# Performance work log

Measured on AMD Instinct MI355X. Metric: run time of the kernel, lower is better.

Reference implementation:

```python
import jax, jax.numpy as jnp
import numpy as np
from jax import lax

HOPS = 3
B, L, D = 16, 512, 768


def _softmask(x, mask):
    # x: [B,L,L] scores, mask: [B,L] {0,1} floats. Scaled masked softmax per RACL softmask_2d.
    x = x - jnp.max(x, axis=-1, keepdims=True)
    y = jnp.exp(x) * mask[:, None, :]          # mask keys
    att = y / (jnp.sum(y, axis=-1, keepdims=True) + 1e-10)
    return att * mask[:, :, None]              # mask queries


def _conv1d(x, w, b):
    # x: [B,L,D]; w: [D_out, D_in, 3]; conv over L with padding 1 (same length).
    out = lax.conv_general_dilated(jnp.transpose(x, (0, 2, 1)), w, (1,), [(1, 1)],
                                   dimension_numbers=('NCH', 'OIH', 'NCH'))
    return jnp.transpose(out + b[None, :, None], (0, 2, 1))


def _l2norm(x):
    # F.normalize(p=2, dim=-1) with eps=1e-12 (clamp_min)
    return x / jnp.maximum(jnp.linalg.norm(x, axis=-1, keepdims=True), 1e-12)


def setup_inputs() -> dict:
    key = jax.random.key(0)
    ks = jax.random.split(key, 8)
    inputs = jax.random.normal(ks[0], (B, L, D), dtype=jnp.float32)
    mask = jnp.ones((B, L), dtype=jnp.float32)
    conv_w = jax.random.normal(ks[1], (HOPS, D, D, 3), dtype=jnp.float32) * 0.02
    conv_b = jax.random.normal(ks[2], (HOPS, D), dtype=jnp.float32) * 0.02
    pool_w1 = jax.random.normal(ks[3], (D, D), dtype=jnp.float32) * 0.02
    pool_b1 = jax.random.normal(ks[4], (D,), dtype=jnp.float32) * 0.02
    pool_w2 = jax.random.normal(ks[5], (D,), dtype=jnp.float32) * 0.02
    pool_b2 = jax.random.normal(ks[6], (1,), dtype=jnp.float32) * 0.02
    position = jnp.zeros((B, L), dtype=jnp.int64)  # unused by the module
    return {"inputs": inputs, "mask": mask, "conv_w": conv_w, "conv_b": conv_b,
            "pool_w1": pool_w1, "pool_b1": pool_b1, "pool_w2": pool_w2,
            "pool_b2": pool_b2, "position": position}


def reference(inputs, mask, conv_w, conv_b, pool_w1, pool_b1, pool_w2, pool_b2, position):
    att_out = []
    # hop 0: raw (un-normalized) similarity on inputs
    see = jnp.einsum('bld,bmd->blm', inputs, inputs)
    att_out.append(jnp.einsum('blm,bmd->bld', _softmask(see, mask), inputs)[:, :, None, :])
    cur = inputs
    for h in range(HOPS):
        conv = jax.nn.relu(_conv1d(cur, conv_w[h], conv_b[h]))  # dropout = identity (eval)
        n = _l2norm(conv)
        att = _softmask(jnp.einsum('bld,bmd->blm', n, n), mask)  # cosine-sim attention
        att_out.append(jnp.einsum('blm,bmd->bld', att, conv)[:, :, None, :])
        cur = conv
    result = jnp.concatenate(att_out, axis=-2)  # [B,L,HOPS+1,D]
    hidden = jnp.tanh(jnp.einsum('blhd,de->blhe', result, pool_w1) + pool_b1)
    scores = jnp.einsum('blhd,d->blh', hidden, pool_w2) + pool_b2  # [B,L,HOPS+1]
    att_w = jax.nn.softmax(scores, axis=-1)
    weighted = jnp.einsum('blh,blhd->bld', att_w, result)
    return cur, weighted
```

## Files before the change

### kernel.cpp

```cpp
#include <hip/hip_runtime.h>
#include <math.h>

#define B_ 16
#define L_ 512
#define D_ 768
#define HOPS_ 3
#define LK 64

typedef __attribute__((ext_vector_type(8))) short s16x8;
typedef __attribute__((ext_vector_type(4))) short s16x4;
typedef __attribute__((ext_vector_type(4))) float f32x4;

typedef __attribute__((address_space(1))) const unsigned gu32;
typedef __attribute__((address_space(3))) unsigned lu32;

__device__ __forceinline__ void gl16(const void* g, void* l) {
  __builtin_amdgcn_global_load_lds((gu32*)g, (lu32*)l, 16, 0, 0);
}

__device__ __forceinline__ short f2bf(float f) {
  unsigned u = __float_as_uint(f);
  unsigned r = (u + 0x7fffu + ((u >> 16) & 1u)) >> 16;
  return (short)r;
}
__device__ __forceinline__ float bf2f(short s) {
  unsigned u = ((unsigned)(unsigned short)s) << 16;
  return __uint_as_float(u);
}
__device__ __forceinline__ float tanh_fast(float x) {
  float e = __expf(2.f * x);
  return 1.f - 2.f / (e + 1.f);
}

__device__ __forceinline__ s16x8* lds_slot(short (*T)[LK], int row, int slot) {
  return (s16x8*)&T[row][(slot ^ (row & 7)) * 8];
}

__device__ __forceinline__ void mfma4(short (*As)[LK], short (*Bs)[LK],
                                      f32x4 acc[4][4], int wr, int wc, int lq, int lr) {
#pragma unroll
  for (int ks = 0; ks < 2; ++ks) {
    int sl = ks * 4 + lq;
    s16x8 av[4], bv[4];
#pragma unroll
    for (int m = 0; m < 4; ++m) av[m] = *lds_slot(As, wr * 64 + m * 16 + lr, sl);
#pragma unroll
    for (int n = 0; n < 4; ++n) bv[n] = *lds_slot(Bs, wc * 64 + n * 16 + lr, sl);
#pragma unroll
    for (int m = 0; m < 4; ++m)
#pragma unroll
      for (int n = 0; n < 4; ++n)
        acc[m][n] = __builtin_amdgcn_mfma_f32_16x16x32_bf16(av[m], bv[n], acc[m][n], 0, 0, 0);
  }
}

__device__ __forceinline__ void mfma2(short (*As)[LK], short (*Bs)[LK],
                                      f32x4 acc[2][4], int wr, int wc, int lq, int lr) {
#pragma unroll
  for (int ks = 0; ks < 2; ++ks) {
    int sl = ks * 4 + lq;
    s16x8 av[2], bv[4];
#pragma unroll
    for (int m = 0; m < 2; ++m) av[m] = *lds_slot(As, wr * 32 + m * 16 + lr, sl);
#pragma unroll
    for (int n = 0; n < 4; ++n) bv[n] = *lds_slot(Bs, wc * 64 + n * 16 + lr, sl);
#pragma unroll
    for (int m = 0; m < 2; ++m)
#pragma unroll
      for (int n = 0; n < 4; ++n)
        acc[m][n] = __builtin_amdgcn_mfma_f32_16x16x32_bf16(av[m], bv[n], acc[m][n], 0, 0, 0);
  }
}

__device__ __forceinline__ int xcd_remap(int bid, int n) {
  return (bid & 7) * (n >> 3) + (bid >> 3);
}

template <int SPLIT>
__global__ __launch_bounds__(256) void k_sim_mfma(const short* __restrict__ X,
                                                  float* __restrict__ Sout) {
  int wg = xcd_remap(blockIdx.x, gridDim.x);
  int jb = wg & 3, ib = (wg >> 2) & 7, b = wg >> 5;
  int i0 = ib * 64, j0 = jb * 128;
  const int ld = SPLIT ? 1536 : D_;
  const short* Xb = X + (size_t)b * L_ * ld;
  int t = threadIdx.x, lane = t & 63, wid = t >> 6;
  int wr = wid >> 1, wc = wid & 1, lq = lane >> 4, lr = lane & 15;
  __shared__ short As[64][LK];
  __shared__ short Bs[128][LK];
  f32x4 acc[2][4];
#pragma unroll
  for (int m = 0; m < 2; ++m)
#pragma unroll
    for (int n = 0; n < 4; ++n) acc[m][n] = (f32x4){0.f, 0.f, 0.f, 0.f};
  int lrow = lane >> 3;
  int sw = ((lane & 7) ^ lrow) * 8;
  const short* apg[2];
  const short* bpg[4];
#pragma unroll
  for (int j = 0; j < 2; ++j)
    apg[j] = Xb + (size_t)(i0 + wid * 16 + j * 8 + lrow) * ld + sw;
#pragma unroll
  for (int j = 0; j < 4; ++j)
    bpg[j] = Xb + (size_t)(j0 + wid * 32 + j * 8 + lrow) * ld + sw;

  const int K = SPLIT ? 2304 : D_;
  for (int k0 = 0; k0 < K; k0 += LK) {
    int seg = SPLIT ? (k0 / 768) : 0;
    int kl = k0 - seg * 768;
    int ak = kl + ((SPLIT && seg == 1) ? 768 : 0);
    int bk = kl + ((SPLIT && seg == 2) ? 768 : 0);
#pragma unroll
    for (int j = 0; j < 2; ++j) gl16(apg[j] + ak, &As[wid * 16 + j * 8][0]);
#pragma unroll
    for (int j = 0; j < 4; ++j) gl16(bpg[j] + bk, &Bs[wid * 32 + j * 8][0]);
    __syncthreads();
    mfma2(As, Bs, acc, wr, wc, lq, lr);
    __syncthreads();
  }
  float* Cb = Sout + (size_t)b * L_ * L_;
#pragma unroll
  for (int m = 0; m < 2; ++m)
#pragma unroll
    for (int n = 0; n < 4; ++n)
#pragma unroll
      for (int rr = 0; rr < 4; ++rr)
        Cb[(size_t)(i0 + wr * 32 + m * 16 + 4 * lq + rr) * L_ +
           (j0 + wc * 64 + n * 16 + lr)] = acc[m][n][rr];
}

template <int WF32>
__global__ __launch_bounds__(256) void k_conv_mfma(const short* __restrict__ X, int ldx,
                                                   const short* __restrict__ Wt2,
                                                   const float* __restrict__ bias,
                                                   short* __restrict__ Ybf,
                                                   float* __restrict__ Yf,
                                                   float* __restrict__ rnsq,
                                                   const short* __restrict__ zbuf,
                                                   short* __restrict__ Vt) {
  int wg = xcd_remap(blockIdx.x, gridDim.x);
  int ob = wg % 6;
  int m_ = wg / 6;
  int b = m_ >> 2, l0 = (m_ & 3) * 128, o0 = ob * 128;
  const short* Xb = X + (size_t)b * L_ * ldx;
  int t = threadIdx.x, lane = t & 63, wid = t >> 6;
  int wr = wid >> 1, wc = wid & 1, lq = lane >> 4, lr = lane & 15;
  __shared__ short smem[17408];
  short (*As)[LK] = (short(*)[LK])smem;
  short (*Bs)[LK] = (short(*)[LK])(smem + 128 * LK);
  f32x4 acc[4][4];
#pragma unroll
  for (int m = 0; m < 4; ++m)
#pragma unroll
    for (int n = 0; n < 4; ++n) acc[m][n] = (f32x4){0.f, 0.f, 0.f, 0.f};
  int lrow = lane >> 3;
  int sw = ((lane & 7) ^ lrow) * 8;
  int arow[4];
  const short* bpg[4];
#pragma unroll
  for (int j = 0; j < 4; ++j) {
    arow[j] = l0 + wid * 32 + j * 8 + lrow;
    bpg[j] = Wt2 + (size_t)(o0 + wid * 32 + j * 8 + lrow) * (3 * D_) + sw;
  }
  const short* zp = zbuf + sw;

  for (int k0 = 0; k0 < 3 * D_; k0 += LK) {
    int tap = k0 / D_;
    int kl = k0 - tap * D_;
#pragma unroll
    for (int j = 0; j < 4; ++j) {
      int l = arow[j] + tap - 1;
      const short* src =
          ((unsigned)l < (unsigned)L_) ? Xb + (size_t)l * ldx + kl + sw : zp;
      gl16(src, &As[wid * 32 + j * 8][0]);
    }
#pragma unroll
    for (int j = 0; j < 4; ++j) gl16(bpg[j] + k0, &Bs[wid * 32 + j * 8][0]);
    __syncthreads();
    mfma4(As, Bs, acc, wr, wc, lq, lr);
    __syncthreads();
  }
  float bv[4];
#pragma unroll
  for (int n = 0; n < 4; ++n) bv[n] = bias[o0 + wc * 64 + n * 16 + lr];
#pragma unroll
  for (int m = 0; m < 4; ++m)
#pragma unroll
    for (int n = 0; n < 4; ++n)
#pragma unroll
      for (int rr = 0; rr < 4; ++rr)
        acc[m][n][rr] = fmaxf(acc[m][n][rr] + bv[n], 0.f);
#pragma unroll
  for (int m = 0; m < 4; ++m)
#pragma unroll
    for (int rr = 0; rr < 4; ++rr) {
      int l = l0 + wr * 64 + m * 16 + 4 * lq + rr;
      size_t rowoff = ((size_t)b * L_ + l) * D_;
      float ss = 0.f;
#pragma unroll
      for (int n = 0; n < 4; ++n) {
        int o = o0 + wc * 64 + n * 16 + lr;
        float v = acc[m][n][rr];
        Ybf[rowoff + o] = f2bf(v);
        if (WF32) Yf[rowoff + o] = v;
        ss += v * v;
      }
      ss += __shfl_xor(ss, 1);
      ss += __shfl_xor(ss, 2);
      ss += __shfl_xor(ss, 4);
      ss += __shfl_xor(ss, 8);
      if (lr == 0) atomicAdd(&rnsq[(size_t)b * L_ + l], ss);
    }
  short (*T)[136] = (short(*)[136])smem;
#pragma unroll
  for (int m = 0; m < 4; ++m)
#pragma unroll
    for (int n = 0; n < 4; ++n) {
      int o_ = wc * 64 + n * 16 + lr;
      int lb = wr * 64 + m * 16 + 4 * lq;
      s16x4 pk;
#pragma unroll
      for (int rr = 0; rr < 4; ++rr) pk[rr] = f2bf(acc[m][n][rr]);
      *(s16x4*)&T[o_][lb] = pk;
    }
  __syncthreads();
  short* Vtb = Vt + (size_t)b * D_ * L_;
#pragma unroll
  for (int p = 0; p < 8; ++p) {
    int dl = p * 16 + (t >> 4), lc = (t & 15) * 8;
    s16x8 q = *(const s16x8*)&T[dl][lc];
    *(s16x8*)&Vtb[(size_t)(o0 + dl) * L_ + l0 + lc] = q;
  }
}

__global__ __launch_bounds__(256) void k_att_mfma(const short* __restrict__ P,
                                                  const short* __restrict__ Vt,
                                                  short* __restrict__ Rb, int hop) {
  int wg = xcd_remap(blockIdx.x, gridDim.x);
  int db = wg % 6;
  int r2 = wg / 6;
  int b = r2 >> 2, i0 = (r2 & 3) * 128, d0 = db * 128;
  const short* Pb = P + (size_t)b * L_ * L_;
  const short* Vb = Vt + (size_t)b * D_ * L_;
  int t = threadIdx.x, lane = t & 63, wid = t >> 6;
  int wr = wid >> 1, wc = wid & 1, lq = lane >> 4, lr = lane & 15;
  __shared__ short As[128][LK];
  __shared__ short Bs[128][LK];
  f32x4 acc[4][4];
#pragma unroll
  for (int m = 0; m < 4; ++m)
#pragma unroll
    for (int n = 0; n < 4; ++n) acc[m][n] = (f32x4){0.f, 0.f, 0.f, 0.f};
  int lrow = lane >> 3;
  int sw = ((lane & 7) ^ lrow) * 8;
  const short* apg[4];
  const short* bpg[4];
#pragma unroll
  for (int j = 0; j < 4; ++j) {
    apg[j] = Pb + (size_t)(i0 + wid * 32 + j * 8 + lrow) * L_ + sw;
    bpg[j] = Vb + (size_t)(d0 + wid * 32 + j * 8 + lrow) * L_ + sw;
  }
  for (int k0 = 0; k0 < L_; k0 += LK) {
#pragma unroll
    for (int j = 0; j < 4; ++j) gl16(apg[j] + k0, &As[wid * 32 + j * 8][0]);
#pragma unroll
    for (int j = 0; j < 4; ++j) gl16(bpg[j] + k0, &Bs[wid * 32 + j * 8][0]);
    __syncthreads();
    mfma4(As, Bs, acc, wr, wc, lq, lr);
    __syncthreads();
  }
#pragma unroll
  for (int m = 0; m < 4; ++m)
#pragma unroll
    for (int n = 0; n < 4; ++n)
#pragma unroll
      for (int rr = 0; rr < 4; ++rr) {
        int i = i0 + wr * 64 + m * 16 + 4 * lq + rr;
        int d = d0 + wc * 64 + n * 16 + lr;
        Rb[((size_t)(b * L_ + i) * 4 + hop) * D_ + d] = f2bf(acc[m][n][rr]);
      }
}

__global__ __launch_bounds__(256) void k_pool_mfma(const short* __restrict__ Rb,
                                                   const short* __restrict__ W1t,
                                                   const float* __restrict__ b1,
                                                   const float* __restrict__ w2,
                                                   float* __restrict__ ps) {
  int wg = xcd_remap(blockIdx.x, gridDim.x);
  int eb = wg % 6;
  int r0 = (wg / 6) * 128, e0 = eb * 128;
  int t = threadIdx.x, lane = t & 63, wid = t >> 6;
  int wr = wid >> 1, wc = wid & 1, lq = lane >> 4, lr = lane & 15;
  __shared__ short As[128][LK];
  __shared__ short Bs[128][LK];
  f32x4 acc[4][4];
#pragma unroll
  for (int m = 0; m < 4; ++m)
#pragma unroll
    for (int n = 0; n < 4; ++n) acc[m][n] = (f32x4){0.f, 0.f, 0.f, 0.f};
  int lrow = lane >> 3;
  int sw = ((lane & 7) ^ lrow) * 8;
  const short* apg[4];
  const short* bpg[4];
#pragma unroll
  for (int j = 0; j < 4; ++j) {
    apg[j] = Rb + (size_t)(r0 + wid * 32 + j * 8 + lrow) * D_ + sw;
    bpg[j] = W1t + (size_t)(e0 + wid * 32 + j * 8 + lrow) * D_ + sw;
  }
  for (int k0 = 0; k0 < D_; k0 += LK) {
#pragma unroll
    for (int j = 0; j < 4; ++j) gl16(apg[j] + k0, &As[wid * 32 + j * 8][0]);
#pragma unroll
    for (int j = 0; j < 4; ++j) gl16(bpg[j] + k0, &Bs[wid * 32 + j * 8][0]);
    __syncthreads();
    mfma4(As, Bs, acc, wr, wc, lq, lr);
    __syncthreads();
  }
  float b1v[4], w2v[4];
#pragma unroll
  for (int n = 0; n < 4; ++n) {
    int e = e0 + wc * 64 + n * 16 + lr;
    b1v[n] = b1[e];
    w2v[n] = w2[e];
  }
#pragma unroll
  for (int m = 0; m < 4; ++m)
#pragma unroll
    for (int rr = 0; rr < 4; ++rr) {
      float p = 0.f;
#pragma unroll
      for (int n = 0; n < 4; ++n) p += tanh_fast(acc[m][n][rr] + b1v[n]) * w2v[n];
      p += __shfl_xor(p, 1);
      p += __shfl_xor(p, 2);
      p += __shfl_xor(p, 4);
      p += __shfl_xor(p, 8);
      if (lr == 0) atomicAdd(&ps[r0 + wr * 64 + m * 16 + 4 * lq + rr], p);
    }
}

__global__ __launch_bounds__(256) void k_prep2(const float* __restrict__ in,
                                               short* __restrict__ Xs,
                                               short* __restrict__ Vt) {
  int l0 = blockIdx.x * 32, d0 = blockIdx.y * 32, b = blockIdx.z;
  __shared__ short tile[32][40];
  int r = threadIdx.x >> 5, c = threadIdx.x & 31;
  const float* ib = in + ((size_t)b * L_ + l0) * D_ + d0;
#pragma unroll
  for (int i = 0; i < 4; ++i) {
    int rr = r + 8 * i;
    float x = ib[(size_t)rr * D_ + c];
    short hi = f2bf(x);
    short lo = f2bf(x - bf2f(hi));
    size_t bl = (size_t)b * L_ + l0 + rr;
    Xs[bl * 1536 + d0 + c] = hi;
    Xs[bl * 1536 + 768 + d0 + c] = lo;
    tile[c][rr] = hi;
  }
  __syncthreads();
  int dl = threadIdx.x >> 3, lc = (threadIdx.x & 7) * 4;
  s16x4 q = *(const s16x4*)&tile[dl][lc];
  *(s16x4*)&Vt[((size_t)b * D_ + d0 + dl) * L_ + l0 + lc] = q;
}

__global__ void k_wprep(const float* __restrict__ w, const float* __restrict__ W1,
                        short* __restrict__ Wt2, short* __restrict__ W1t) {
  size_t idx = (size_t)blockIdx.x * 256 + threadIdx.x;
  const size_t tot1 = (size_t)HOPS_ * D_ * 3 * D_;
  if (idx < tot1) {
    int i = (int)(idx % D_);
    size_t tmp = idx / D_;
    int kk = (int)(tmp % 3);
    tmp /= 3;
    int o = (int)(tmp % D_);
    int h = (int)(tmp / D_);
    Wt2[idx] = f2bf(w[(((size_t)h * D_ + o) * D_ + i) * 3 + kk]);
  } else {
    size_t i2 = idx - tot1;
    if (i2 >= (size_t)D_ * D_) return;
    int e = (int)(i2 / D_), d = (int)(i2 % D_);
    W1t[i2] = f2bf(W1[(size_t)d * D_ + e]);
  }
}

template <int NORM>
__global__ __launch_bounds__(256) void k_softmask3(const float* __restrict__ S,
                                                   const float* __restrict__ mask,
                                                   const float* __restrict__ rsq,
                                                   short* __restrict__ P) {
  int b = blockIdx.y;
  int i = blockIdx.x * 4 + (threadIdx.x >> 6);
  int l = threadIdx.x & 63;
  const float* row = S + ((size_t)b * L_ + i) * L_;
  const float* mb = mask + (size_t)b * L_;
  float v[8], mk[8];
  {
    float4 s0 = ((const float4*)row)[l * 2];
    float4 s1 = ((const float4*)row)[l * 2 + 1];
    float4 m0 = ((const float4*)mb)[l * 2];
    float4 m1 = ((const float4*)mb)[l * 2 + 1];
    v[0] = s0.x; v[1] = s0.y; v[2] = s0.z; v[3] = s0.w;
    v[4] = s1.x; v[5] = s1.y; v[6] = s1.z; v[7] = s1.w;
    mk[0] = m0.x; mk[1] = m0.y; mk[2] = m0.z; mk[3] = m0.w;
    mk[4] = m1.x; mk[5] = m1.y; mk[6] = m1.z; mk[7] = m1.w;
  }
  if (NORM) {
    float ri = 1.f / fmaxf(sqrtf(rsq[(size_t)b * L_ + i]), 1e-12f);
    const float4* rq = (const float4*)(rsq + (size_t)b * L_);
    float4 q0 = rq[l * 2], q1 = rq[l * 2 + 1];
    float qq[8] = {q0.x, q0.y, q0.z, q0.w, q1.x, q1.y, q1.z, q1.w};
#pragma unroll
    for (int e = 0; e < 8; ++e) v[e] *= ri / fmaxf(sqrtf(qq[e]), 1e-12f);
  }
  float m = v[0];
#pragma unroll
  for (int e = 1; e < 8; ++e) m = fmaxf(m, v[e]);
#pragma unroll
  for (int s = 1; s < 64; s <<= 1) m = fmaxf(m, __shfl_xor(m, s));
  float y[8], sum = 0.f;
#pragma unroll
  for (int e = 0; e < 8; ++e) {
    y[e] = __expf(v[e] - m) * mk[e];
    sum += y[e];
  }
#pragma unroll
  for (int s = 1; s < 64; s <<= 1) sum += __shfl_xor(sum, s);
  float inv = mb[i] / (sum + 1e-10f);
  s16x8 pk;
#pragma unroll
  for (int e = 0; e < 8; ++e) pk[e] = f2bf(y[e] * inv);
  ((s16x8*)(P + ((size_t)b * L_ + i) * L_))[l] = pk;
}

__global__ __launch_bounds__(256) void k_weighted2(const short* __restrict__ Rb,
                                                   const float* __restrict__ ps,
                                                   float* __restrict__ out) {
  int b = blockIdx.y, l = blockIdx.x;
  size_t bl = (size_t)b * L_ + l;
  const float* p = ps + bl * 4;
  float s0 = p[0], s1 = p[1], s2 = p[2], s3 = p[3];
  float m = fmaxf(fmaxf(s0, s1), fmaxf(s2, s3));
  float e0 = __expf(s0 - m), e1 = __expf(s1 - m), e2 = __expf(s2 - m),
        e3 = __expf(s3 - m);
  float inv = 1.f / (e0 + e1 + e2 + e3);
  e0 *= inv; e1 *= inv; e2 *= inv; e3 *= inv;
  const short* Rrow = Rb + bl * 4 * D_;
  float* orow = out + bl * D_;
  for (int d = threadIdx.x; d < D_; d += 256) {
    orow[d] = e0 * bf2f(Rrow[d]) + e1 * bf2f(Rrow[D_ + d]) +
              e2 * bf2f(Rrow[2 * D_ + d]) + e3 * bf2f(Rrow[3 * D_ + d]);
  }
}

extern "C" void kernel_launch(void* const* d_in, const int* in_sizes, int n_in,
                              void* d_out, int out_size, void* d_ws, size_t ws_size,
                              hipStream_t stream) {
  const float* inputs  = (const float*)d_in[0];
  const float* mask    = (const float*)d_in[1];
  const float* conv_w  = (const float*)d_in[2];
  const float* conv_b  = (const float*)d_in[3];
  const float* pool_w1 = (const float*)d_in[4];
  const float* pool_b1 = (const float*)d_in[5];
  const float* pool_w2 = (const float*)d_in[6];
  float* out = (float*)d_out;

  const size_t BLD = (size_t)B_ * L_ * D_;
  const size_t BLL = (size_t)B_ * L_ * L_;
  const size_t BL  = (size_t)B_ * L_;

  char* w = (char*)d_ws;
  short* Xs   = (short*)w; w += (size_t)2 * BLD * 2;
  short* Wt2  = (short*)w; w += (size_t)HOPS_ * 3 * D_ * D_ * 2;
  short* W1t  = (short*)w; w += (size_t)D_ * D_ * 2;
  float* S    = (float*)w; w += BLL * 4;
  short* Pb   = (short*)w; w += BLL * 2;
  short* YbfA = (short*)w; w += BLD * 2;
  short* YbfB = (short*)w; w += BLD * 2;
  short* Vt   = (short*)w; w += BLD * 2;
  short* Rb   = (short*)w; w += 4 * BLD * 2;
  float* ps   = (float*)w; w += BL * 4 * 4;
  float* rnsq = (float*)w; w += BL * 3 * 4;
  short* zbuf = (short*)w; w += 1024;
  const size_t zero_bytes = BL * 4 * 4 + BL * 3 * 4 + 1024;

  hipMemsetAsync(ps, 0, zero_bytes, stream);

  dim3 gpre(L_ / 32, D_ / 32, B_);
  dim3 gsm(L_ / 4, B_);
  dim3 grow(L_, B_);
  const int GSIM = (L_ / 64) * (L_ / 128) * B_;
  const int GCONV = (D_ / 128) * (L_ / 128) * B_;
  const int GATT = GCONV;
  const int GPOOL = (D_ / 128) * (4 * B_ * L_ / 128);
  const size_t wtot = (size_t)HOPS_ * D_ * 3 * D_ + (size_t)D_ * D_;

  k_prep2<<<gpre, 256, 0, stream>>>(inputs, Xs, Vt);
  k_wprep<<<dim3((unsigned)((wtot + 255) / 256)), 256, 0, stream>>>(conv_w, pool_w1,
                                                                     Wt2, W1t);

  k_sim_mfma<1><<<GSIM, 256, 0, stream>>>(Xs, S);
  k_softmask3<0><<<gsm, 256, 0, stream>>>(S, mask, nullptr, Pb);
  k_att_mfma<<<GATT, 256, 0, stream>>>(Pb, Vt, Rb, 0);

  const short* cur = Xs;
  int ldc = 1536;
  for (int h = 0; h < HOPS_; ++h) {
    short* cv = (h & 1) ? YbfB : YbfA;
    const short* Wh = Wt2 + (size_t)h * 3 * D_ * D_;
    const float* bh = conv_b + (size_t)h * D_;
    float* rq = rnsq + (size_t)h * BL;
    if (h == HOPS_ - 1)
      k_conv_mfma<1><<<GCONV, 256, 0, stream>>>(cur, ldc, Wh, bh, cv, out, rq, zbuf, Vt);
    else
      k_conv_mfma<0><<<GCONV, 256, 0, stream>>>(cur, ldc, Wh, bh, cv, nullptr, rq, zbuf, Vt);
    k_sim_mfma<0><<<GSIM, 256, 0, stream>>>(cv, S);
    k_softmask3<1><<<gsm, 256, 0, stream>>>(S, mask, rq, Pb);
    k_att_mfma<<<GATT, 256, 0, stream>>>(Pb, Vt, Rb, h + 1);
    cur = cv;
    ldc = D_;
  }

  k_pool_mfma<<<GPOOL, 256, 0, stream>>>(Rb, W1t, pool_b1, pool_w2, ps);
  k_weighted2<<<grow, 256, 0, stream>>>(Rb, ps, out + BLD);
}
```

Measured before the change: 483.0 us.

## Fuse similarity GEMM with masked softmax into one kernel producing bf16 probabilities

Replaces the separate similarity GEMM (which wrote fp32 scores to global memory) and the row-softmax kernel with one kernel. Each 512-thread block computes full 32x512 score rows and does the max/sum reductions in registers and LDS, then writes bf16 probabilities directly. This removes the fp32 score round trip and four kernel launches. The cost is fewer, larger blocks (256 total) with a K-step of 32 and more barriers, which may reduce occupancy and MFMA efficiency. The final weighted-sum kernel is also vectorised to process two rows per block with 16-byte loads.

```diff
diff --git a/kernel.cpp b/kernel.cpp
--- a/kernel.cpp
+++ b/kernel.cpp
@@ -54,79 +54,159 @@
   }
 }
 
-__device__ __forceinline__ void mfma2(short (*As)[LK], short (*Bs)[LK],
-                                      f32x4 acc[2][4], int wr, int wc, int lq, int lr) {
-#pragma unroll
-  for (int ks = 0; ks < 2; ++ks) {
-    int sl = ks * 4 + lq;
-    s16x8 av[2], bv[4];
-#pragma unroll
-    for (int m = 0; m < 2; ++m) av[m] = *lds_slot(As, wr * 32 + m * 16 + lr, sl);
-#pragma unroll
-    for (int n = 0; n < 4; ++n) bv[n] = *lds_slot(Bs, wc * 64 + n * 16 + lr, sl);
-#pragma unroll
-    for (int m = 0; m < 2; ++m)
-#pragma unroll
-      for (int n = 0; n < 4; ++n)
-        acc[m][n] = __builtin_amdgcn_mfma_f32_16x16x32_bf16(av[m], bv[n], acc[m][n], 0, 0, 0);
-  }
-}
-
 __device__ __forceinline__ int xcd_remap(int bid, int n) {
   return (bid & 7) * (n >> 3) + (bid >> 3);
 }
 
-template <int SPLIT>
-__global__ __launch_bounds__(256) void k_sim_mfma(const short* __restrict__ X,
-                                                  float* __restrict__ Sout) {
+template <int SPLIT, int NORM>
+__global__ __launch_bounds__(512) void k_simsm(const short* __restrict__ X,
+                                               const float* __restrict__ mask,
+                                               const float* __restrict__ rsq,
+                                               short* __restrict__ P) {
   int wg = xcd_remap(blockIdx.x, gridDim.x);
-  int jb = wg & 3, ib = (wg >> 2) & 7, b = wg >> 5;
-  int i0 = ib * 64, j0 = jb * 128;
+  int ib = wg & 15, b = wg >> 4;
+  int i0 = ib * 32;
   const int ld = SPLIT ? 1536 : D_;
   const short* Xb = X + (size_t)b * L_ * ld;
-  int t = threadIdx.x, lane = t & 63, wid = t >> 6;
-  int wr = wid >> 1, wc = wid & 1, lq = lane >> 4, lr = lane & 15;
-  __shared__ short As[64][LK];
-  __shared__ short Bs[128][LK];
+  int t = threadIdx.x, lane = t & 63, w = t >> 6;
+  int lq = lane >> 4, lr = lane & 15;
+  __shared__ __align__(16) short smem[17408];
+  short (*As)[32] = (short(*)[32])smem;
+  short (*Bs)[32] = (short(*)[32])(smem + 1024);
   f32x4 acc[2][4];
 #pragma unroll
   for (int m = 0; m < 2; ++m)
 #pragma unroll
     for (int n = 0; n < 4; ++n) acc[m][n] = (f32x4){0.f, 0.f, 0.f, 0.f};
-  int lrow = lane >> 3;
-  int sw = ((lane & 7) ^ lrow) * 8;
-  const short* apg[2];
-  const short* bpg[4];
-#pragma unroll
-  for (int j = 0; j < 2; ++j)
-    apg[j] = Xb + (size_t)(i0 + wid * 16 + j * 8 + lrow) * ld + sw;
-#pragma unroll
-  for (int j = 0; j < 4; ++j)
-    bpg[j] = Xb + (size_t)(j0 + wid * 32 + j * 8 + lrow) * ld + sw;
+
+  int rl = lane >> 2;
+  int ss = ((lane & 3) ^ ((lane >> 3) & 3)) * 8;
+  int wa = (w < 2) ? w : 0;
+  const short* asrc = Xb + (size_t)(i0 + wa * 16 + rl) * ld + ss;
+  short* adst = &As[wa * 16][0];
+  const short* bsrc[4];
+  short* bdst[4];
+#pragma unroll
+  for (int jj = 0; jj < 4; ++jj) {
+    int r0 = jj * 128 + w * 16;
+    bsrc[jj] = Xb + (size_t)(r0 + rl) * ld + ss;
+    bdst[jj] = &Bs[r0][0];
+  }
+  int so = (lq ^ ((lr >> 1) & 3)) * 8;
 
   const int K = SPLIT ? 2304 : D_;
-  for (int k0 = 0; k0 < K; k0 += LK) {
+  for (int k0 = 0; k0 < K; k0 += 32) {
     int seg = SPLIT ? (k0 / 768) : 0;
     int kl = k0 - seg * 768;
     int ak = kl + ((SPLIT && seg == 1) ? 768 : 0);
     int bk = kl + ((SPLIT && seg == 2) ? 768 : 0);
-#pragma unroll
-    for (int j = 0; j < 2; ++j) gl16(apg[j] + ak, &As[wid * 16 + j * 8][0]);
-#pragma unroll
-    for (int j = 0; j < 4; ++j) gl16(bpg[j] + bk, &Bs[wid * 32 + j * 8][0]);
-    __syncthreads();
-    mfma2(As, Bs, acc, wr, wc, lq, lr);
-    __syncthreads();
-  }
-  float* Cb = Sout + (size_t)b * L_ * L_;
+    if (w < 2) gl16(asrc + ak, adst);
+#pragma unroll
+    for (int jj = 0; jj < 4; ++jj) gl16(bsrc[jj] + bk, bdst[jj]);
+    __syncthreads();
+    s16x8 av[2], bv[4];
+#pragma unroll
+    for (int m = 0; m < 2; ++m) av[m] = *(const s16x8*)&As[m * 16 + lr][so];
+#pragma unroll
+    for (int n = 0; n < 4; ++n) bv[n] = *(const s16x8*)&Bs[w * 64 + n * 16 + lr][so];
+#pragma unroll
+    for (int m = 0; m < 2; ++m)
+#pragma unroll
+      for (int n = 0; n < 4; ++n)
+        acc[m][n] = __builtin_amdgcn_mfma_f32_16x16x32_bf16(av[m], bv[n], acc[m][n], 0, 0, 0);
+    __syncthreads();
+  }
+
+  const float* mb = mask + (size_t)b * L_;
+  const float* rqb = rsq + (size_t)b * L_;
+  float mk_j[4], inv_rj[4];
+#pragma unroll
+  for (int n = 0; n < 4; ++n) {
+    int col = w * 64 + n * 16 + lr;
+    mk_j[n] = mb[col];
+    if (NORM) inv_rj[n] = 1.f / fmaxf(sqrtf(rqb[col]), 1e-12f);
+  }
+  float mk_i[2][4], inv_ri[2][4], rmax[2][4];
 #pragma unroll
   for (int m = 0; m < 2; ++m)
 #pragma unroll
-    for (int n = 0; n < 4; ++n)
+    for (int rr = 0; rr < 4; ++rr) {
+      int row = m * 16 + lq * 4 + rr;
+      mk_i[m][rr] = mb[i0 + row];
+      if (NORM) inv_ri[m][rr] = 1.f / fmaxf(sqrtf(rqb[i0 + row]), 1e-12f);
+      float vmx = -3.4e38f;
+#pragma unroll
+      for (int n = 0; n < 4; ++n) {
+        float v = acc[m][n][rr];
+        if (NORM) v *= inv_ri[m][rr] * inv_rj[n];
+        acc[m][n][rr] = v;
+        vmx = fmaxf(vmx, v);
+      }
+#pragma unroll
+      for (int s = 1; s < 16; s <<= 1) vmx = fmaxf(vmx, __shfl_xor(vmx, s));
+      rmax[m][rr] = vmx;
+    }
+  float* red = (float*)smem;
+  float* rowred = red + 256;
+  if (lr == 0) {
+#pragma unroll
+    for (int m = 0; m < 2; ++m)
 #pragma unroll
       for (int rr = 0; rr < 4; ++rr)
-        Cb[(size_t)(i0 + wr * 32 + m * 16 + 4 * lq + rr) * L_ +
-           (j0 + wc * 64 + n * 16 + lr)] = acc[m][n][rr];
+        red[w * 32 + m * 16 + lq * 4 + rr] = rmax[m][rr];
+  }
+  __syncthreads();
+  if (t < 32) {
+    float mx = red[t];
+#pragma unroll
+    for (int ww = 1; ww < 8; ++ww) mx = fmaxf(mx, red[ww * 32 + t]);
+    rowred[t] = mx;
+  }
+  __syncthreads();
+  float rsum[2][4];
+#pragma unroll
+  for (int m = 0; m < 2; ++m)
+#pragma unroll
+    for (int rr = 0; rr < 4; ++rr) {
+      float M = rowred[m * 16 + lq * 4 + rr];
+      float s = 0.f;
+#pragma unroll
+      for (int n = 0; n < 4; ++n) {
+        float y = __expf(acc[m][n][rr] - M) * mk_j[n];
+        acc[m][n][rr] = y;
+        s += y;
+      }
+#pragma unroll
+      for (int sh = 1; sh < 16; sh <<= 1) s += __shfl_xor(s, sh);
+      rsum[m][rr] = s;
+    }
+  __syncthreads();
+  if (lr == 0) {
+#pragma unroll
+    for (int m = 0; m < 2; ++m)
+#pragma unroll
+      for (int rr = 0; rr < 4; ++rr)
+        red[w * 32 + m * 16 + lq * 4 + rr] = rsum[m][rr];
+  }
+  __syncthreads();
+  if (t < 32) {
+    float s = red[t];
+#pragma unroll
+    for (int ww = 1; ww < 8; ++ww) s += red[ww * 32 + t];
+    rowred[t] = s;
+  }
+  __syncthreads();
+  short* Pb = P + ((size_t)b * L_ + i0) * L_;
+#pragma unroll
+  for (int m = 0; m < 2; ++m)
+#pragma unroll
+    for (int rr = 0; rr < 4; ++rr) {
+      int row = m * 16 + lq * 4 + rr;
+      float inv = mk_i[m][rr] / (rowred[row] + 1e-10f);
+#pragma unroll
+      for (int n = 0; n < 4; ++n)
+        Pb[(size_t)row * L_ + w * 64 + n * 16 + lr] = f2bf(acc[m][n][rr] * inv);
+    }
 }
 
 template <int WF32>
@@ -145,7 +225,7 @@
   const short* Xb = X + (size_t)b * L_ * ldx;
   int t = threadIdx.x, lane = t & 63, wid = t >> 6;
   int wr = wid >> 1, wc = wid & 1, lq = lane >> 4, lr = lane & 15;
-  __shared__ short smem[17408];
+  __shared__ __align__(16) short smem[17408];
   short (*As)[LK] = (short(*)[LK])smem;
   short (*Bs)[LK] = (short(*)[LK])(smem + 128 * LK);
   f32x4 acc[4][4];
@@ -244,8 +324,8 @@
   const short* Vb = Vt + (size_t)b * D_ * L_;
   int t = threadIdx.x, lane = t & 63, wid = t >> 6;
   int wr = wid >> 1, wc = wid & 1, lq = lane >> 4, lr = lane & 15;
-  __shared__ short As[128][LK];
-  __shared__ short Bs[128][LK];
+  __shared__ __align__(16) short As[128][LK];
+  __shared__ __align__(16) short Bs[128][LK];
   f32x4 acc[4][4];
 #pragma unroll
   for (int m = 0; m < 4; ++m)
@@ -291,8 +371,8 @@
   int r0 = (wg / 6) * 128, e0 = eb * 128;
   int t = threadIdx.x, lane = t & 63, wid = t >> 6;
   int wr = wid >> 1, wc = wid & 1, lq = lane >> 4, lr = lane & 15;
-  __shared__ short As[128][LK];
-  __shared__ short Bs[128][LK];
+  __shared__ __align__(16) short As[128][LK];
+  __shared__ __align__(16) short Bs[128][LK];
   f32x4 acc[4][4];
 #pragma unroll
   for (int m = 0; m < 4; ++m)
@@ -382,60 +462,13 @@
   }
 }
 
-template <int NORM>
-__global__ __launch_bounds__(256) void k_softmask3(const float* __restrict__ S,
-                                                   const float* __restrict__ mask,
-                                                   const float* __restrict__ rsq,
-                                                   short* __restrict__ P) {
-  int b = blockIdx.y;
-  int i = blockIdx.x * 4 + (threadIdx.x >> 6);
-  int l = threadIdx.x & 63;
-  const float* row = S + ((size_t)b * L_ + i) * L_;
-  const float* mb = mask + (size_t)b * L_;
-  float v[8], mk[8];
-  {
-    float4 s0 = ((const float4*)row)[l * 2];
-    float4 s1 = ((const float4*)row)[l * 2 + 1];
-    float4 m0 = ((const float4*)mb)[l * 2];
-    float4 m1 = ((const float4*)mb)[l * 2 + 1];
-    v[0] = s0.x; v[1] = s0.y; v[2] = s0.z; v[3] = s0.w;
-    v[4] = s1.x; v[5] = s1.y; v[6] = s1.z; v[7] = s1.w;
-    mk[0] = m0.x; mk[1] = m0.y; mk[2] = m0.z; mk[3] = m0.w;
-    mk[4] = m1.x; mk[5] = m1.y; mk[6] = m1.z; mk[7] = m1.w;
-  }
-  if (NORM) {
-    float ri = 1.f / fmaxf(sqrtf(rsq[(size_t)b * L_ + i]), 1e-12f);
-    const float4* rq = (const float4*)(rsq + (size_t)b * L_);
-    float4 q0 = rq[l * 2], q1 = rq[l * 2 + 1];
-    float qq[8] = {q0.x, q0.y, q0.z, q0.w, q1.x, q1.y, q1.z, q1.w};
-#pragma unroll
-    for (int e = 0; e < 8; ++e) v[e] *= ri / fmaxf(sqrtf(qq[e]), 1e-12f);
-  }
-  float m = v[0];
-#pragma unroll
-  for (int e = 1; e < 8; ++e) m = fmaxf(m, v[e]);
-#pragma unroll
-  for (int s = 1; s < 64; s <<= 1) m = fmaxf(m, __shfl_xor(m, s));
-  float y[8], sum = 0.f;
-#pragma unroll
-  for (int e = 0; e < 8; ++e) {
-    y[e] = __expf(v[e] - m) * mk[e];
-    sum += y[e];
-  }
-#pragma unroll
-  for (int s = 1; s < 64; s <<= 1) sum += __shfl_xor(sum, s);
-  float inv = mb[i] / (sum + 1e-10f);
-  s16x8 pk;
-#pragma unroll
-  for (int e = 0; e < 8; ++e) pk[e] = f2bf(y[e] * inv);
-  ((s16x8*)(P + ((size_t)b * L_ + i) * L_))[l] = pk;
-}
-
 __global__ __launch_bounds__(256) void k_weighted2(const short* __restrict__ Rb,
                                                    const float* __restrict__ ps,
                                                    float* __restrict__ out) {
-  int b = blockIdx.y, l = blockIdx.x;
-  size_t bl = (size_t)b * L_ + l;
+  if (threadIdx.x >= 192) return;
+  int rowl = threadIdx.x / 96;
+  int ln = threadIdx.x % 96;
+  size_t bl = (size_t)blockIdx.x * 2 + rowl;
   const float* p = ps + bl * 4;
   float s0 = p[0], s1 = p[1], s2 = p[2], s3 = p[3];
   float m = fmaxf(fmaxf(s0, s1), fmaxf(s2, s3));
@@ -444,11 +477,22 @@
   float inv = 1.f / (e0 + e1 + e2 + e3);
   e0 *= inv; e1 *= inv; e2 *= inv; e3 *= inv;
   const short* Rrow = Rb + bl * 4 * D_;
-  float* orow = out + bl * D_;
-  for (int d = threadIdx.x; d < D_; d += 256) {
-    orow[d] = e0 * bf2f(Rrow[d]) + e1 * bf2f(Rrow[D_ + d]) +
-              e2 * bf2f(Rrow[2 * D_ + d]) + e3 * bf2f(Rrow[3 * D_ + d]);
-  }
+  int d = ln * 8;
+  s16x8 r0 = *(const s16x8*)&Rrow[d];
+  s16x8 r1 = *(const s16x8*)&Rrow[D_ + d];
+  s16x8 r2 = *(const s16x8*)&Rrow[2 * D_ + d];
+  s16x8 r3 = *(const s16x8*)&Rrow[3 * D_ + d];
+  float* orow = out + bl * D_ + d;
+  float4 o0, o1;
+  float* ov[2] = {&o0.x, &o1.x};
+#pragma unroll
+  for (int e = 0; e < 8; ++e) {
+    float v = e0 * bf2f(r0[e]) + e1 * bf2f(r1[e]) + e2 * bf2f(r2[e]) +
+              e3 * bf2f(r3[e]);
+    ov[e >> 2][e & 3] = v;
+  }
+  ((float4*)orow)[0] = o0;
+  ((float4*)orow)[1] = o1;
 }
 
 extern "C" void kernel_launch(void* const* d_in, const int* in_sizes, int n_in,
@@ -471,7 +515,6 @@
   short* Xs   = (short*)w; w += (size_t)2 * BLD * 2;
   short* Wt2  = (short*)w; w += (size_t)HOPS_ * 3 * D_ * D_ * 2;
   short* W1t  = (short*)w; w += (size_t)D_ * D_ * 2;
-  float* S    = (float*)w; w += BLL * 4;
   short* Pb   = (short*)w; w += BLL * 2;
   short* YbfA = (short*)w; w += BLD * 2;
   short* YbfB = (short*)w; w += BLD * 2;
@@ -485,9 +528,7 @@
   hipMemsetAsync(ps, 0, zero_bytes, stream);
 
   dim3 gpre(L_ / 32, D_ / 32, B_);
-  dim3 gsm(L_ / 4, B_);
-  dim3 grow(L_, B_);
-  const int GSIM = (L_ / 64) * (L_ / 128) * B_;
+  const int GSIM = (L_ / 32) * B_;
   const int GCONV = (D_ / 128) * (L_ / 128) * B_;
   const int GATT = GCONV;
   const int GPOOL = (D_ / 128) * (4 * B_ * L_ / 128);
@@ -497,8 +538,7 @@
   k_wprep<<<dim3((unsigned)((wtot + 255) / 256)), 256, 0, stream>>>(conv_w, pool_w1,
                                                                      Wt2, W1t);
 
-  k_sim_mfma<1><<<GSIM, 256, 0, stream>>>(Xs, S);
-  k_softmask3<0><<<gsm, 256, 0, stream>>>(S, mask, nullptr, Pb);
+  k_simsm<1, 0><<<GSIM, 512, 0, stream>>>(Xs, mask, rnsq, Pb);
   k_att_mfma<<<GATT, 256, 0, stream>>>(Pb, Vt, Rb, 0);
 
   const short* cur = Xs;
@@ -512,13 +552,12 @@
       k_conv_mfma<1><<<GCONV, 256, 0, stream>>>(cur, ldc, Wh, bh, cv, out, rq, zbuf, Vt);
     else
       k_conv_mfma<0><<<GCONV, 256, 0, stream>>>(cur, ldc, Wh, bh, cv, nullptr, rq, zbuf, Vt);
-    k_sim_mfma<0><<<GSIM, 256, 0, stream>>>(cv, S);
-    k_softmask3<1><<<gsm, 256, 0, stream>>>(S, mask, rq, Pb);
+    k_simsm<0, 1><<<GSIM, 512, 0, stream>>>(cv, mask, rq, Pb);
     k_att_mfma<<<GATT, 256, 0, stream>>>(Pb, Vt, Rb, h + 1);
     cur = cv;
     ldc = D_;
   }
 
   k_pool_mfma<<<GPOOL, 256, 0, stream>>>(Rb, W1t, pool_b1, pool_w2, ps);
-  k_weighted2<<<grow, 256, 0, stream>>>(Rb, ps, out + BLD);
-}
+  k_weighted2<<<dim3((unsigned)(BL / 2)), 256, 0, stream>>>(Rb, ps, out + BLD);
+}
```

After: 527.4 us. 1.09x slower.
